# Kernel tuning notes

Measured on AMD Instinct MI355X. Metric: run time of the kernel, lower is better.

## Reference

```python
import jax, jax.numpy as jnp
import numpy as np
import math

NUM_HEADS = 8
WINDOW = 8  # stage=1


def _windowed_attention(q, kv, Wq, bq, Wk, bk, Wv, bv, Wo, bo):
    B, N, C = q.shape
    H = W = int(math.isqrt(N))
    nh, ws = NUM_HEADS, WINDOW
    hd = C // nh
    scale = hd ** -0.5

    qp = q @ Wq + bq   # (B, N, C)
    kp = kv @ Wk + bk
    vp = kv @ Wv + bv

    def to_windows(x):
        # (B, N, C) -> (B, nh, nWh*nWw, ws*ws, hd)
        x = x.reshape(B, H // ws, ws, W // ws, ws, nh, hd)
        x = x.transpose(0, 5, 1, 3, 2, 4, 6)  # B, nh, nWh, nWw, ws, ws, hd
        return x.reshape(B, nh, (H // ws) * (W // ws), ws * ws, hd)

    qw = to_windows(qp)
    kw = to_windows(kp)
    vw = to_windows(vp)

    attn = jnp.einsum('bhnqd,bhnkd->bhnqk', qw, kw) * scale
    attn = jax.nn.softmax(attn.astype(jnp.float32), axis=-1).astype(qw.dtype)
    ow = jnp.einsum('bhnqk,bhnkd->bhnqd', attn, vw)

    # window reverse: (B, nh, nW, ws*ws, hd) -> (B, N, C)
    ow = ow.reshape(B, nh, H // ws, W // ws, ws, ws, hd)
    ow = ow.transpose(0, 2, 4, 3, 5, 1, 6)  # B, nWh, ws, nWw, ws, nh, hd
    x = ow.reshape(B, N, C)

    return x @ Wo + bo


def setup_inputs() -> dict:
    key = jax.random.key(0)
    ks = jax.random.split(key, 7)
    B, N, C = 4, 16384, 256
    s = 1.0 / math.sqrt(C)
    return {
        'q': jax.random.normal(ks[0], (B, N, C), jnp.float32),
        'kv': jax.random.normal(ks[1], (B, N, C), jnp.float32),
        'Wq': jax.random.normal(ks[2], (C, C), jnp.float32) * s,
        'bq': jnp.zeros((C,), jnp.float32),
        'Wk': jax.random.normal(ks[3], (C, C), jnp.float32) * s,
        'bk': jnp.zeros((C,), jnp.float32),
        'Wv': jax.random.normal(ks[4], (C, C), jnp.float32) * s,
        'bv': jnp.zeros((C,), jnp.float32),
        'Wo': jax.random.normal(ks[5], (C, C), jnp.float32) * s,
        'bo': jnp.zeros((C,), jnp.float32),
    }


def reference(q, kv, Wq, bq, Wk, bk, Wv, bv, Wo, bo):
    return _windowed_attention(q, kv, Wq, bq, Wk, bk, Wv, bv, Wo, bo)
```

## Files before the change

### kernel.cpp

```cpp
#include <hip/hip_runtime.h>
#include <hip/hip_bf16.h>

typedef __bf16 bf16;
typedef __bf16 bf16x8 __attribute__((ext_vector_type(8)));
typedef float  f32x4  __attribute__((ext_vector_type(4)));

#define DEVINL __device__ __forceinline__

DEVINL void gll16(const void* g, void* l) {
  __builtin_amdgcn_global_load_lds(
      (const __attribute__((address_space(1))) unsigned int*)g,
      (__attribute__((address_space(3))) unsigned int*)l, 16, 0, 0);
}

__global__ void k_prep(const float* __restrict__ Wq, const float* __restrict__ Wk,
                       const float* __restrict__ Wv, const float* __restrict__ Wo,
                       bf16* __restrict__ wtq_h, bf16* __restrict__ wtq_l,
                       bf16* __restrict__ wtkv_h, bf16* __restrict__ wtkv_l,
                       bf16* __restrict__ wto_h, bf16* __restrict__ wto_l) {
  const int k = blockIdx.x;
  const int n = threadIdx.x;
  const int m = blockIdx.y;
  const float* src = (m == 0) ? Wq : (m == 1) ? Wk : (m == 2) ? Wv : Wo;
  bf16* dh = (m == 0) ? wtq_h : (m == 3) ? wto_h : (m == 1) ? wtkv_h : (wtkv_h + 256 * 256);
  bf16* dl = (m == 0) ? wtq_l : (m == 3) ? wto_l : (m == 1) ? wtkv_l : (wtkv_l + 256 * 256);
  const float v = src[k * 256 + n];
  const bf16 h = (bf16)v;
  dh[n * 256 + k] = h;
  dl[n * 256 + k] = (bf16)(v - (float)h);
}

template <bool ABF16, bool OUTF32>
__global__ __launch_bounds__(256) void k_gemm3(
    const void* __restrict__ Aptr,
    const bf16* __restrict__ Wth, const bf16* __restrict__ Wtl,
    const float* __restrict__ bias0, const float* __restrict__ bias1,
    void* __restrict__ out0, void* __restrict__ out1) {
  __shared__ __align__(16) bf16 Ash[128 * 32];
  __shared__ __align__(16) bf16 Asl[128 * 32];
  __shared__ __align__(16) bf16 Bsh[128 * 32];
  __shared__ __align__(16) bf16 Bsl[128 * 32];

  const int tid = threadIdx.x;
  const int lane = tid & 63;
  const int wave = tid >> 6;
  const int m0 = blockIdx.x * 128;
  const int n0 = blockIdx.y * 128;
  const int mw = (wave >> 1) * 64;
  const int nw = (wave & 1) * 64;
  const int lm = lane & 15;
  const int lq = lane >> 4;

  f32x4 acc[4][4];
#pragma unroll
  for (int i = 0; i < 4; ++i)
#pragma unroll
    for (int j = 0; j < 4; ++j) acc[i][j] = (f32x4)0.0f;

  const int c0 = wave * 128 + lane;
  const int c1 = c0 + 64;
  const int rB0 = c0 >> 2, oB0 = (c0 & 3) * 8;
  const int rB1 = c1 >> 2, oB1 = (c1 & 3) * 8;

  const int rowA = tid >> 1;
  const int halfA = (tid & 1) * 16;

  for (int k0 = 0; k0 < 256; k0 += 32) {
    gll16(Wth + (size_t)(n0 + rB0) * 256 + k0 + oB0, &Bsh[c0 * 8]);
    gll16(Wth + (size_t)(n0 + rB1) * 256 + k0 + oB1, &Bsh[c1 * 8]);
    gll16(Wtl + (size_t)(n0 + rB0) * 256 + k0 + oB0, &Bsl[c0 * 8]);
    gll16(Wtl + (size_t)(n0 + rB1) * 256 + k0 + oB1, &Bsl[c1 * 8]);

    if (ABF16) {
      const bf16* Ab = (const bf16*)Aptr;
      gll16(Ab + (size_t)(m0 + rB0) * 256 + k0 + oB0, &Ash[c0 * 8]);
      gll16(Ab + (size_t)(m0 + rB1) * 256 + k0 + oB1, &Ash[c1 * 8]);
    } else {
      const float* Af = (const float*)Aptr;
      const float* src = Af + (size_t)(m0 + rowA) * 256 + k0 + halfA;
      float4 f0 = *(const float4*)(src);
      float4 f1 = *(const float4*)(src + 4);
      float4 f2 = *(const float4*)(src + 8);
      float4 f3 = *(const float4*)(src + 12);
      bf16x8 h0, l0, h1, l1;
      const float fa[16] = {f0.x, f0.y, f0.z, f0.w, f1.x, f1.y, f1.z, f1.w,
                            f2.x, f2.y, f2.z, f2.w, f3.x, f3.y, f3.z, f3.w};
#pragma unroll
      for (int j = 0; j < 8; ++j) {
        bf16 h = (bf16)fa[j];
        h0[j] = h;
        l0[j] = (bf16)(fa[j] - (float)h);
      }
#pragma unroll
      for (int j = 0; j < 8; ++j) {
        bf16 h = (bf16)fa[8 + j];
        h1[j] = h;
        l1[j] = (bf16)(fa[8 + j] - (float)h);
      }
      const int o = rowA * 32 + halfA;
      *(bf16x8*)&Ash[o] = h0;
      *(bf16x8*)&Ash[o + 8] = h1;
      *(bf16x8*)&Asl[o] = l0;
      *(bf16x8*)&Asl[o + 8] = l1;
    }
    __syncthreads();

    bf16x8 avh[4], bvh[4], bvl[4];
#pragma unroll
    for (int t = 0; t < 4; ++t)
      avh[t] = *(const bf16x8*)&Ash[(mw + t * 16 + lm) * 32 + lq * 8];
#pragma unroll
    for (int t = 0; t < 4; ++t) {
      bvh[t] = *(const bf16x8*)&Bsh[(nw + t * 16 + lm) * 32 + lq * 8];
      bvl[t] = *(const bf16x8*)&Bsl[(nw + t * 16 + lm) * 32 + lq * 8];
    }
#pragma unroll
    for (int i = 0; i < 4; ++i)
#pragma unroll
      for (int j = 0; j < 4; ++j) {
        acc[i][j] = __builtin_amdgcn_mfma_f32_16x16x32_bf16(avh[i], bvh[j], acc[i][j], 0, 0, 0);
        acc[i][j] = __builtin_amdgcn_mfma_f32_16x16x32_bf16(avh[i], bvl[j], acc[i][j], 0, 0, 0);
      }
    if (!ABF16) {
      bf16x8 avl[4];
#pragma unroll
      for (int t = 0; t < 4; ++t)
        avl[t] = *(const bf16x8*)&Asl[(mw + t * 16 + lm) * 32 + lq * 8];
#pragma unroll
      for (int i = 0; i < 4; ++i)
#pragma unroll
        for (int j = 0; j < 4; ++j)
          acc[i][j] = __builtin_amdgcn_mfma_f32_16x16x32_bf16(avl[i], bvh[j], acc[i][j], 0, 0, 0);
    }
    __syncthreads();
  }

#pragma unroll
  for (int i = 0; i < 4; ++i) {
#pragma unroll
    for (int j = 0; j < 4; ++j) {
      const int n_g = n0 + nw + j * 16 + lm;
      const bool hi = (n_g >= 256);
      const float* bp = hi ? bias1 : bias0;
      const int nc = n_g & 255;
      const float bval = bp[nc];
#pragma unroll
      for (int r = 0; r < 4; ++r) {
        const int m_g = m0 + mw + i * 16 + lq * 4 + r;
        const float v = acc[i][j][r] + bval;
        if (OUTF32) {
          float* op = hi ? (float*)out1 : (float*)out0;
          op[(size_t)m_g * 256 + nc] = v;
        } else {
          bf16* op = hi ? (bf16*)out1 : (bf16*)out0;
          op[(size_t)m_g * 256 + nc] = (bf16)v;
        }
      }
    }
  }
}

__global__ __launch_bounds__(256) void k_attn(
    const bf16* __restrict__ qp, const bf16* __restrict__ kp,
    const bf16* __restrict__ vp, bf16* __restrict__ ao) {
  __shared__ __align__(16) bf16 smem[3 * 64 * 136];
  bf16* Qs = smem;
  bf16* Ks = smem + 64 * 136;
  bf16* Vs = smem + 2 * 64 * 136;
  bf16* Ps = smem;
  bf16* Os = Vs;

  const int tid = threadIdx.x;
  const int lane = tid & 63;
  const int hl = tid >> 6;
  const int bw = blockIdx.x;
  const int b = bw >> 8;
  const int w = bw & 255;
  const int wy = w >> 4, wx = w & 15;
  const int ch0 = blockIdx.y * 128;

#pragma unroll
  for (int i = 0; i < 4; ++i) {
    const int c = i * 256 + tid;
    const int t = c >> 4;
    const int off = (c & 15) * 8;
    const int ty = t >> 3, tx = t & 7;
    const size_t gr = ((size_t)(b * 128 + wy * 8 + ty)) * 128 + wx * 8 + tx;
    const size_t gi = gr * 256 + ch0 + off;
    const int li = t * 136 + off;
    *(uint4*)&Qs[li] = *(const uint4*)&qp[gi];
    *(uint4*)&Ks[li] = *(const uint4*)&kp[gi];
    *(uint4*)&Vs[li] = *(const uint4*)&vp[gi];
  }
  __syncthreads();

  const int chh = hl * 32;
  const int lm = lane & 15;
  const int lq = lane >> 4;

  bf16x8 qa[4], kb[4];
#pragma unroll
  for (int t = 0; t < 4; ++t)
    qa[t] = *(const bf16x8*)&Qs[(t * 16 + lm) * 136 + chh + lq * 8];
#pragma unroll
  for (int t = 0; t < 4; ++t)
    kb[t] = *(const bf16x8*)&Ks[(t * 16 + lm) * 136 + chh + lq * 8];

  f32x4 s[4][4];
#pragma unroll
  for (int i = 0; i < 4; ++i)
#pragma unroll
    for (int j = 0; j < 4; ++j) s[i][j] = (f32x4)0.0f;
#pragma unroll
  for (int i = 0; i < 4; ++i)
#pragma unroll
    for (int j = 0; j < 4; ++j)
      s[i][j] = __builtin_amdgcn_mfma_f32_16x16x32_bf16(qa[i], kb[j], s[i][j], 0, 0, 0);

  const float scale = 0.17677669529663687f;
  float rl[4][4];
#pragma unroll
  for (int mt = 0; mt < 4; ++mt) {
#pragma unroll
    for (int r = 0; r < 4; ++r) {
      float mx = fmaxf(fmaxf(s[mt][0][r], s[mt][1][r]), fmaxf(s[mt][2][r], s[mt][3][r]));
      mx = fmaxf(mx, __shfl_xor(mx, 1));
      mx = fmaxf(mx, __shfl_xor(mx, 2));
      mx = fmaxf(mx, __shfl_xor(mx, 4));
      mx = fmaxf(mx, __shfl_xor(mx, 8));
      float sum = 0.f;
#pragma unroll
      for (int nt = 0; nt < 4; ++nt) {
        const float p = __expf((s[mt][nt][r] - mx) * scale);
        s[mt][nt][r] = p;
        sum += p;
      }
      sum += __shfl_xor(sum, 1);
      sum += __shfl_xor(sum, 2);
      sum += __shfl_xor(sum, 4);
      sum += __shfl_xor(sum, 8);
      rl[mt][r] = 1.0f / sum;
    }
  }

  __syncthreads();

  bf16* Ph = Ps + hl * 4096;
#pragma unroll
  for (int mt = 0; mt < 4; ++mt)
#pragma unroll
    for (int nt = 0; nt < 4; ++nt)
#pragma unroll
      for (int r = 0; r < 4; ++r) {
        const int qrow = mt * 16 + lq * 4 + r;
        const int kcol = nt * 16 + lm;
        Ph[qrow * 64 + (((kcol >> 3) ^ (qrow & 7)) << 3) + (kcol & 7)] = (bf16)s[mt][nt][r];
      }

  f32x4 o[4][2];
#pragma unroll
  for (int i = 0; i < 4; ++i) { o[i][0] = (f32x4)0.0f; o[i][1] = (f32x4)0.0f; }
#pragma unroll
  for (int ks = 0; ks < 2; ++ks) {
    bf16x8 pa[4];
#pragma unroll
    for (int mt = 0; mt < 4; ++mt) {
      const int qrow = mt * 16 + lm;
      const int g = ks * 4 + lq;
      pa[mt] = *(const bf16x8*)&Ph[qrow * 64 + ((g ^ (qrow & 7)) << 3)];
    }
    bf16x8 vbf[2];
#pragma unroll
    for (int ntd = 0; ntd < 2; ++ntd) {
      const int d = ntd * 16 + lm;
      bf16x8 tv;
#pragma unroll
      for (int j = 0; j < 8; ++j)
        tv[j] = Vs[(ks * 32 + lq * 8 + j) * 136 + chh + d];
      vbf[ntd] = tv;
    }
#pragma unroll
    for (int mt = 0; mt < 4; ++mt)
#pragma unroll
      for (int ntd = 0; ntd < 2; ++ntd)
        o[mt][ntd] = __builtin_amdgcn_mfma_f32_16x16x32_bf16(pa[mt], vbf[ntd], o[mt][ntd], 0, 0, 0);
  }

  __syncthreads();

#pragma unroll
  for (int mt = 0; mt < 4; ++mt)
#pragma unroll
    for (int ntd = 0; ntd < 2; ++ntd)
#pragma unroll
      for (int r = 0; r < 4; ++r) {
        const int qrow = mt * 16 + lq * 4 + r;
        const int d = ntd * 16 + lm;
        Os[qrow * 136 + chh + d] = (bf16)(o[mt][ntd][r] * rl[mt][r]);
      }
  __syncthreads();

#pragma unroll
  for (int i = 0; i < 4; ++i) {
    const int c = i * 256 + tid;
    const int t = c >> 4;
    const int off = (c & 15) * 8;
    const int ty = t >> 3, tx = t & 7;
    const size_t gr = ((size_t)(b * 128 + wy * 8 + ty)) * 128 + wx * 8 + tx;
    *(uint4*)&ao[gr * 256 + ch0 + off] = *(const uint4*)&Os[t * 136 + off];
  }
}

extern "C" void kernel_launch(void* const* d_in, const int* in_sizes, int n_in,
                              void* d_out, int out_size, void* d_ws, size_t ws_size,
                              hipStream_t stream) {
  const float* q  = (const float*)d_in[0];
  const float* kv = (const float*)d_in[1];
  const float* Wq = (const float*)d_in[2];
  const float* bq = (const float*)d_in[3];
  const float* Wk = (const float*)d_in[4];
  const float* bk = (const float*)d_in[5];
  const float* Wv = (const float*)d_in[6];
  const float* bv = (const float*)d_in[7];
  const float* Wo = (const float*)d_in[8];
  const float* bo = (const float*)d_in[9];
  float* out = (float*)d_out;

  char* ws = (char*)d_ws;
  bf16* wtq_h  = (bf16*)(ws + 0);
  bf16* wtq_l  = (bf16*)(ws + 131072);
  bf16* wtkv_h = (bf16*)(ws + 262144);
  bf16* wtkv_l = (bf16*)(ws + 524288);
  bf16* wto_h  = (bf16*)(ws + 786432);
  bf16* wto_l  = (bf16*)(ws + 917504);
  const size_t PLANE = (size_t)65536 * 256 * 2;
  bf16* qp = (bf16*)(ws + 1048576);
  bf16* kp = (bf16*)(ws + 1048576 + PLANE);
  bf16* vp = (bf16*)(ws + 1048576 + 2 * PLANE);
  bf16* ao = (bf16*)(ws + 1048576 + 3 * PLANE);
  if (ws_size < 1048576 + 4 * PLANE) return;

  k_prep<<<dim3(256, 4), 256, 0, stream>>>(Wq, Wk, Wv, Wo, wtq_h, wtq_l,
                                           wtkv_h, wtkv_l, wto_h, wto_l);
  k_gemm3<false, false><<<dim3(512, 2), 256, 0, stream>>>(
      (const void*)q, wtq_h, wtq_l, bq, bq, (void*)qp, (void*)qp);
  k_gemm3<false, false><<<dim3(512, 4), 256, 0, stream>>>(
      (const void*)kv, wtkv_h, wtkv_l, bk, bv, (void*)kp, (void*)vp);
  k_attn<<<dim3(1024, 2), 256, 0, stream>>>(qp, kp, vp, ao);
  k_gemm3<true, true><<<dim3(512, 2), 256, 0, stream>>>(
      (const void*)ao, wto_h, wto_l, bo, bo, (void*)out, (void*)out);
}
```

Baseline: 323.6 us.

## Fuse QKV projections, drop activation low-part split, use 64-row tiles with XCD mapping

Replaces the templated GEMM with a fused Q/K/V projection kernel and a dedicated output projection kernel. The fp32 activations are now rounded to a single bf16 term, removing the low-part split and one third of the MFMAs. Tiles shrink to 64 rows, and block indices are remapped so neighbouring rows spread across XCDs, with higher occupancy hints. This trades some accuracy in the projections for less compute and fewer launches.

After: 329.4 us. About the same (+1.8%).

```diff
diff --git a/kernel.cpp b/kernel.cpp
--- a/kernel.cpp
+++ b/kernel.cpp
@@ -11,6 +11,13 @@
   __builtin_amdgcn_global_load_lds(
       (const __attribute__((address_space(1))) unsigned int*)g,
       (__attribute__((address_space(3))) unsigned int*)l, 16, 0, 0);
+}
+
+DEVINL bf16x8 cvt_hi(const float4& a, const float4& b) {
+  bf16x8 h;
+  h[0] = (bf16)a.x; h[1] = (bf16)a.y; h[2] = (bf16)a.z; h[3] = (bf16)a.w;
+  h[4] = (bf16)b.x; h[5] = (bf16)b.y; h[6] = (bf16)b.z; h[7] = (bf16)b.w;
+  return h;
 }
 
 __global__ void k_prep(const float* __restrict__ Wq, const float* __restrict__ Wk,
@@ -30,131 +37,174 @@
   dl[n * 256 + k] = (bf16)(v - (float)h);
 }
 
-template <bool ABF16, bool OUTF32>
-__global__ __launch_bounds__(256) void k_gemm3(
-    const void* __restrict__ Aptr,
-    const bf16* __restrict__ Wth, const bf16* __restrict__ Wtl,
-    const float* __restrict__ bias0, const float* __restrict__ bias1,
-    void* __restrict__ out0, void* __restrict__ out1) {
-  __shared__ __align__(16) bf16 Ash[128 * 32];
-  __shared__ __align__(16) bf16 Asl[128 * 32];
+__global__ __launch_bounds__(256, 4) void k_qkv(
+    const float* __restrict__ q, const float* __restrict__ kv,
+    const bf16* __restrict__ wtq_h, const bf16* __restrict__ wtq_l,
+    const bf16* __restrict__ wtkv_h, const bf16* __restrict__ wtkv_l,
+    const float* __restrict__ bq, const float* __restrict__ bk,
+    const float* __restrict__ bv,
+    bf16* __restrict__ qp, bf16* __restrict__ kp, bf16* __restrict__ vp) {
+  __shared__ __align__(16) bf16 Ash[64 * 32];
   __shared__ __align__(16) bf16 Bsh[128 * 32];
   __shared__ __align__(16) bf16 Bsl[128 * 32];
+
+  const int g = blockIdx.x;
+  const int xcd = g & 7;
+  const int s = g >> 3;
+  const int nb = s % 6;
+  const int mh = s / 6;
+  const int m0 = (mh * 8 + xcd) * 64;
+
+  const bool isq = (nb < 2);
+  const float* A = isq ? q : kv;
+  const bf16* Wh = isq ? wtq_h : wtkv_h;
+  const bf16* Wl = isq ? wtq_l : wtkv_l;
+  const int n0 = isq ? nb * 128 : (nb - 2) * 128;
 
   const int tid = threadIdx.x;
   const int lane = tid & 63;
   const int wave = tid >> 6;
-  const int m0 = blockIdx.x * 128;
-  const int n0 = blockIdx.y * 128;
-  const int mw = (wave >> 1) * 64;
+  const int mw = (wave >> 1) * 32;
   const int nw = (wave & 1) * 64;
   const int lm = lane & 15;
   const int lq = lane >> 4;
 
-  f32x4 acc[4][4];
-#pragma unroll
-  for (int i = 0; i < 4; ++i)
+  f32x4 acc[2][4];
+#pragma unroll
+  for (int i = 0; i < 2; ++i)
 #pragma unroll
     for (int j = 0; j < 4; ++j) acc[i][j] = (f32x4)0.0f;
 
-  const int c0 = wave * 128 + lane;
-  const int c1 = c0 + 64;
-  const int rB0 = c0 >> 2, oB0 = (c0 & 3) * 8;
-  const int rB1 = c1 >> 2, oB1 = (c1 & 3) * 8;
-
-  const int rowA = tid >> 1;
-  const int halfA = (tid & 1) * 16;
+  const int rB0 = tid >> 2, oB0 = (tid & 3) * 8;
+  const int rB1 = (tid + 256) >> 2, oB1 = oB0;
+  const int rowA = tid >> 2;
+  const int qA = (tid & 3) * 8;
 
   for (int k0 = 0; k0 < 256; k0 += 32) {
-    gll16(Wth + (size_t)(n0 + rB0) * 256 + k0 + oB0, &Bsh[c0 * 8]);
-    gll16(Wth + (size_t)(n0 + rB1) * 256 + k0 + oB1, &Bsh[c1 * 8]);
-    gll16(Wtl + (size_t)(n0 + rB0) * 256 + k0 + oB0, &Bsl[c0 * 8]);
-    gll16(Wtl + (size_t)(n0 + rB1) * 256 + k0 + oB1, &Bsl[c1 * 8]);
-
-    if (ABF16) {
-      const bf16* Ab = (const bf16*)Aptr;
-      gll16(Ab + (size_t)(m0 + rB0) * 256 + k0 + oB0, &Ash[c0 * 8]);
-      gll16(Ab + (size_t)(m0 + rB1) * 256 + k0 + oB1, &Ash[c1 * 8]);
-    } else {
-      const float* Af = (const float*)Aptr;
-      const float* src = Af + (size_t)(m0 + rowA) * 256 + k0 + halfA;
-      float4 f0 = *(const float4*)(src);
-      float4 f1 = *(const float4*)(src + 4);
-      float4 f2 = *(const float4*)(src + 8);
-      float4 f3 = *(const float4*)(src + 12);
-      bf16x8 h0, l0, h1, l1;
-      const float fa[16] = {f0.x, f0.y, f0.z, f0.w, f1.x, f1.y, f1.z, f1.w,
-                            f2.x, f2.y, f2.z, f2.w, f3.x, f3.y, f3.z, f3.w};
-#pragma unroll
-      for (int j = 0; j < 8; ++j) {
-        bf16 h = (bf16)fa[j];
-        h0[j] = h;
-        l0[j] = (bf16)(fa[j] - (float)h);
-      }
-#pragma unroll
-      for (int j = 0; j < 8; ++j) {
-        bf16 h = (bf16)fa[8 + j];
-        h1[j] = h;
-        l1[j] = (bf16)(fa[8 + j] - (float)h);
-      }
-      const int o = rowA * 32 + halfA;
-      *(bf16x8*)&Ash[o] = h0;
-      *(bf16x8*)&Ash[o + 8] = h1;
-      *(bf16x8*)&Asl[o] = l0;
-      *(bf16x8*)&Asl[o + 8] = l1;
-    }
+    gll16(Wh + (size_t)(n0 + rB0) * 256 + k0 + oB0, &Bsh[tid * 8]);
+    gll16(Wh + (size_t)(n0 + rB1) * 256 + k0 + oB1, &Bsh[(tid + 256) * 8]);
+    gll16(Wl + (size_t)(n0 + rB0) * 256 + k0 + oB0, &Bsl[tid * 8]);
+    gll16(Wl + (size_t)(n0 + rB1) * 256 + k0 + oB1, &Bsl[(tid + 256) * 8]);
+
+    const float* src = A + (size_t)(m0 + rowA) * 256 + k0 + qA;
+    const float4 f0 = *(const float4*)(src);
+    const float4 f1 = *(const float4*)(src + 4);
+    *(bf16x8*)&Ash[rowA * 32 + qA] = cvt_hi(f0, f1);
     __syncthreads();
 
-    bf16x8 avh[4], bvh[4], bvl[4];
-#pragma unroll
-    for (int t = 0; t < 4; ++t)
-      avh[t] = *(const bf16x8*)&Ash[(mw + t * 16 + lm) * 32 + lq * 8];
-#pragma unroll
-    for (int t = 0; t < 4; ++t) {
-      bvh[t] = *(const bf16x8*)&Bsh[(nw + t * 16 + lm) * 32 + lq * 8];
-      bvl[t] = *(const bf16x8*)&Bsl[(nw + t * 16 + lm) * 32 + lq * 8];
-    }
-#pragma unroll
-    for (int i = 0; i < 4; ++i)
+    bf16x8 av[2], bh[4], bl[4];
+#pragma unroll
+    for (int t = 0; t < 2; ++t)
+      av[t] = *(const bf16x8*)&Ash[(mw + t * 16 + lm) * 32 + lq * 8];
+#pragma unroll
+    for (int j = 0; j < 4; ++j) {
+      bh[j] = *(const bf16x8*)&Bsh[(nw + j * 16 + lm) * 32 + lq * 8];
+      bl[j] = *(const bf16x8*)&Bsl[(nw + j * 16 + lm) * 32 + lq * 8];
+    }
+#pragma unroll
+    for (int i = 0; i < 2; ++i)
 #pragma unroll
       for (int j = 0; j < 4; ++j) {
-        acc[i][j] = __builtin_amdgcn_mfma_f32_16x16x32_bf16(avh[i], bvh[j], acc[i][j], 0, 0, 0);
-        acc[i][j] = __builtin_amdgcn_mfma_f32_16x16x32_bf16(avh[i], bvl[j], acc[i][j], 0, 0, 0);
-      }
-    if (!ABF16) {
-      bf16x8 avl[4];
-#pragma unroll
-      for (int t = 0; t < 4; ++t)
-        avl[t] = *(const bf16x8*)&Asl[(mw + t * 16 + lm) * 32 + lq * 8];
-#pragma unroll
-      for (int i = 0; i < 4; ++i)
-#pragma unroll
-        for (int j = 0; j < 4; ++j)
-          acc[i][j] = __builtin_amdgcn_mfma_f32_16x16x32_bf16(avl[i], bvh[j], acc[i][j], 0, 0, 0);
-    }
+        acc[i][j] = __builtin_amdgcn_mfma_f32_16x16x32_bf16(av[i], bh[j], acc[i][j], 0, 0, 0);
+        acc[i][j] = __builtin_amdgcn_mfma_f32_16x16x32_bf16(av[i], bl[j], acc[i][j], 0, 0, 0);
+      }
     __syncthreads();
   }
 
 #pragma unroll
-  for (int i = 0; i < 4; ++i) {
+  for (int i = 0; i < 2; ++i) {
 #pragma unroll
     for (int j = 0; j < 4; ++j) {
       const int n_g = n0 + nw + j * 16 + lm;
-      const bool hi = (n_g >= 256);
-      const float* bp = hi ? bias1 : bias0;
-      const int nc = n_g & 255;
-      const float bval = bp[nc];
+      bf16* op;
+      float bval;
+      int nc;
+      if (isq) {
+        op = qp; nc = n_g; bval = bq[n_g];
+      } else if (n_g < 256) {
+        op = kp; nc = n_g; bval = bk[n_g];
+      } else {
+        op = vp; nc = n_g - 256; bval = bv[n_g - 256];
+      }
 #pragma unroll
       for (int r = 0; r < 4; ++r) {
         const int m_g = m0 + mw + i * 16 + lq * 4 + r;
-        const float v = acc[i][j][r] + bval;
-        if (OUTF32) {
-          float* op = hi ? (float*)out1 : (float*)out0;
-          op[(size_t)m_g * 256 + nc] = v;
-        } else {
-          bf16* op = hi ? (bf16*)out1 : (bf16*)out0;
-          op[(size_t)m_g * 256 + nc] = (bf16)v;
-        }
+        op[(size_t)m_g * 256 + nc] = (bf16)(acc[i][j][r] + bval);
+      }
+    }
+  }
+}
+
+__global__ __launch_bounds__(256, 4) void k_oproj(
+    const bf16* __restrict__ A, const bf16* __restrict__ Wh,
+    const bf16* __restrict__ Wl, const float* __restrict__ bias,
+    float* __restrict__ out) {
+  __shared__ __align__(16) bf16 Ash[64 * 32];
+  __shared__ __align__(16) bf16 Bsh[128 * 32];
+  __shared__ __align__(16) bf16 Bsl[128 * 32];
+
+  const int g = blockIdx.x;
+  const int xcd = g & 7;
+  const int s = g >> 3;
+  const int nb = s & 1;
+  const int mh = s >> 1;
+  const int m0 = (mh * 8 + xcd) * 64;
+  const int n0 = nb * 128;
+
+  const int tid = threadIdx.x;
+  const int lane = tid & 63;
+  const int wave = tid >> 6;
+  const int mw = (wave >> 1) * 32;
+  const int nw = (wave & 1) * 64;
+  const int lm = lane & 15;
+  const int lq = lane >> 4;
+
+  f32x4 acc[2][4];
+#pragma unroll
+  for (int i = 0; i < 2; ++i)
+#pragma unroll
+    for (int j = 0; j < 4; ++j) acc[i][j] = (f32x4)0.0f;
+
+  const int rB0 = tid >> 2, oB0 = (tid & 3) * 8;
+  const int rB1 = (tid + 256) >> 2;
+
+  for (int k0 = 0; k0 < 256; k0 += 32) {
+    gll16(Wh + (size_t)(n0 + rB0) * 256 + k0 + oB0, &Bsh[tid * 8]);
+    gll16(Wh + (size_t)(n0 + rB1) * 256 + k0 + oB0, &Bsh[(tid + 256) * 8]);
+    gll16(Wl + (size_t)(n0 + rB0) * 256 + k0 + oB0, &Bsl[tid * 8]);
+    gll16(Wl + (size_t)(n0 + rB1) * 256 + k0 + oB0, &Bsl[(tid + 256) * 8]);
+    gll16(A + (size_t)(m0 + rB0) * 256 + k0 + oB0, &Ash[tid * 8]);
+    __syncthreads();
+
+    bf16x8 av[2], bh[4], bl[4];
+#pragma unroll
+    for (int t = 0; t < 2; ++t)
+      av[t] = *(const bf16x8*)&Ash[(mw + t * 16 + lm) * 32 + lq * 8];
+#pragma unroll
+    for (int j = 0; j < 4; ++j) {
+      bh[j] = *(const bf16x8*)&Bsh[(nw + j * 16 + lm) * 32 + lq * 8];
+      bl[j] = *(const bf16x8*)&Bsl[(nw + j * 16 + lm) * 32 + lq * 8];
+    }
+#pragma unroll
+    for (int i = 0; i < 2; ++i)
+#pragma unroll
+      for (int j = 0; j < 4; ++j) {
+        acc[i][j] = __builtin_amdgcn_mfma_f32_16x16x32_bf16(av[i], bh[j], acc[i][j], 0, 0, 0);
+        acc[i][j] = __builtin_amdgcn_mfma_f32_16x16x32_bf16(av[i], bl[j], acc[i][j], 0, 0, 0);
+      }
+    __syncthreads();
+  }
+
+#pragma unroll
+  for (int i = 0; i < 2; ++i) {
+#pragma unroll
+    for (int j = 0; j < 4; ++j) {
+      const int n_g = n0 + nw + j * 16 + lm;
+      const float bval = bias[n_g];
+#pragma unroll
+      for (int r = 0; r < 4; ++r) {
+        const int m_g = m0 + mw + i * 16 + lq * 4 + r;
+        out[(size_t)m_g * 256 + n_g] = acc[i][j][r] + bval;
       }
     }
   }
@@ -266,8 +316,8 @@
 #pragma unroll
     for (int mt = 0; mt < 4; ++mt) {
       const int qrow = mt * 16 + lm;
-      const int g = ks * 4 + lq;
-      pa[mt] = *(const bf16x8*)&Ph[qrow * 64 + ((g ^ (qrow & 7)) << 3)];
+      const int gsel = ks * 4 + lq;
+      pa[mt] = *(const bf16x8*)&Ph[qrow * 64 + ((gsel ^ (qrow & 7)) << 3)];
     }
     bf16x8 vbf[2];
 #pragma unroll
@@ -342,11 +392,8 @@
 
   k_prep<<<dim3(256, 4), 256, 0, stream>>>(Wq, Wk, Wv, Wo, wtq_h, wtq_l,
                                            wtkv_h, wtkv_l, wto_h, wto_l);
-  k_gemm3<false, false><<<dim3(512, 2), 256, 0, stream>>>(
-      (const void*)q, wtq_h, wtq_l, bq, bq, (void*)qp, (void*)qp);
-  k_gemm3<false, false><<<dim3(512, 4), 256, 0, stream>>>(
-      (const void*)kv, wtkv_h, wtkv_l, bk, bv, (void*)kp, (void*)vp);
+  k_qkv<<<6144, 256, 0, stream>>>(q, kv, wtq_h, wtq_l, wtkv_h, wtkv_l,
+                                  bq, bk, bv, qp, kp, vp);
   k_attn<<<dim3(1024, 2), 256, 0, stream>>>(qp, kp, vp, ao);
-  k_gemm3<true, true><<<dim3(512, 2), 256, 0, stream>>>(
-      (const void*)ao, wto_h, wto_l, bo, bo, (void*)out, (void*)out);
-}
+  k_oproj<<<2048, 256, 0, stream>>>(ao, wto_h, wto_l, bo, out);
+}
```

## Drop split-bf16 compensation in QKV, pre-pack weights, fuse QKV GEMM launches

Applied to the files above, without the earlier changes.

The Q/K/V projections now use plain bf16 inputs and weights instead of the hi/lo split with three MFMAs per tile, and the separate Q and KV GEMMs become one kernel with XCD-aware block mapping. Weights are pre-packed into a tile-contiguous layout so B tiles are staged with straight global_load_lds copies. K is now processed 64 at a time per barrier pair. The output projection keeps compensation only on the weights, as an extra K-range of the packed layout. The intent is to cut MFMA work and launch count, at the cost of lower projection precision that could affect the tolerance check.

Measured after the change: 311.4 us. 1.04x faster.

```diff
diff --git a/kernel.cpp b/kernel.cpp
--- a/kernel.cpp
+++ b/kernel.cpp
@@ -15,149 +15,182 @@
 
 __global__ void k_prep(const float* __restrict__ Wq, const float* __restrict__ Wk,
                        const float* __restrict__ Wv, const float* __restrict__ Wo,
-                       bf16* __restrict__ wtq_h, bf16* __restrict__ wtq_l,
-                       bf16* __restrict__ wtkv_h, bf16* __restrict__ wtkv_l,
-                       bf16* __restrict__ wto_h, bf16* __restrict__ wto_l) {
+                       bf16* __restrict__ packQ, bf16* __restrict__ packO) {
+  const int n = threadIdx.x;
   const int k = blockIdx.x;
-  const int n = threadIdx.x;
   const int m = blockIdx.y;
-  const float* src = (m == 0) ? Wq : (m == 1) ? Wk : (m == 2) ? Wv : Wo;
-  bf16* dh = (m == 0) ? wtq_h : (m == 3) ? wto_h : (m == 1) ? wtkv_h : (wtkv_h + 256 * 256);
-  bf16* dl = (m == 0) ? wtq_l : (m == 3) ? wto_l : (m == 1) ? wtkv_l : (wtkv_l + 256 * 256);
-  const float v = src[k * 256 + n];
-  const bf16 h = (bf16)v;
-  dh[n * 256 + k] = h;
-  dl[n * 256 + k] = (bf16)(v - (float)h);
-}
-
-template <bool ABF16, bool OUTF32>
-__global__ __launch_bounds__(256) void k_gemm3(
-    const void* __restrict__ Aptr,
-    const bf16* __restrict__ Wth, const bf16* __restrict__ Wtl,
-    const float* __restrict__ bias0, const float* __restrict__ bias1,
-    void* __restrict__ out0, void* __restrict__ out1) {
-  __shared__ __align__(16) bf16 Ash[128 * 32];
-  __shared__ __align__(16) bf16 Asl[128 * 32];
-  __shared__ __align__(16) bf16 Bsh[128 * 32];
-  __shared__ __align__(16) bf16 Bsl[128 * 32];
-
-  const int tid = threadIdx.x;
-  const int lane = tid & 63;
-  const int wave = tid >> 6;
-  const int m0 = blockIdx.x * 128;
-  const int n0 = blockIdx.y * 128;
-  const int mw = (wave >> 1) * 64;
-  const int nw = (wave & 1) * 64;
-  const int lm = lane & 15;
-  const int lq = lane >> 4;
+  const int kk = k & 63, iter4 = k >> 6;
+  const int h = kk >> 5, kg = (kk >> 3) & 3, e = k & 7;
+  if (m < 3) {
+    const float* W = (m == 0) ? Wq : (m == 1) ? Wk : Wv;
+    const bf16 v = (bf16)W[k * 256 + n];
+    const int nglob = m * 256 + n;
+    const int tile = nglob >> 7, row = nglob & 127;
+    packQ[(size_t)((tile * 4 + iter4) * 1024 + h * 512 + row * 4 + kg) * 8 + e] = v;
+  } else {
+    const float w = Wo[k * 256 + n];
+    const bf16 hi = (bf16)w;
+    const bf16 v = (m == 3) ? hi : (bf16)(w - (float)hi);
+    const int iter = (m - 3) * 4 + iter4;
+    const int tile = n >> 7, row = n & 127;
+    packO[(size_t)((tile * 8 + iter) * 1024 + h * 512 + row * 4 + kg) * 8 + e] = v;
+  }
+}
+
+__global__ __launch_bounds__(256, 3) void k_qkv(
+    const float* __restrict__ q, const float* __restrict__ kv,
+    const bf16* __restrict__ packQ,
+    const float* __restrict__ bq, const float* __restrict__ bk,
+    const float* __restrict__ bvv,
+    bf16* __restrict__ qp, bf16* __restrict__ kp, bf16* __restrict__ vp) {
+  __shared__ __align__(16) bf16 As[2][128 * 32];
+  __shared__ __align__(16) bf16 Bs[2][128 * 32];
+
+  const int g = blockIdx.x, xcd = g & 7, s = g >> 3;
+  const int nb = s % 6, mh = s / 6;
+  const int m0 = (mh * 8 + xcd) * 128;
+  const float* A = (nb < 2) ? q : kv;
+
+  const int tid = threadIdx.x, lane = tid & 63, wave = tid >> 6;
+  const int mw = (wave >> 1) * 64, nw = (wave & 1) * 64;
+  const int lm = lane & 15, lq = lane >> 4;
 
   f32x4 acc[4][4];
 #pragma unroll
-  for (int i = 0; i < 4; ++i)
-#pragma unroll
-    for (int j = 0; j < 4; ++j) acc[i][j] = (f32x4)0.0f;
-
-  const int c0 = wave * 128 + lane;
-  const int c1 = c0 + 64;
-  const int rB0 = c0 >> 2, oB0 = (c0 & 3) * 8;
-  const int rB1 = c1 >> 2, oB1 = (c1 & 3) * 8;
+  for (int a = 0; a < 4; ++a)
+#pragma unroll
+    for (int b = 0; b < 4; ++b) acc[a][b] = (f32x4)0.0f;
 
   const int rowA = tid >> 1;
-  const int halfA = (tid & 1) * 16;
-
-  for (int k0 = 0; k0 < 256; k0 += 32) {
-    gll16(Wth + (size_t)(n0 + rB0) * 256 + k0 + oB0, &Bsh[c0 * 8]);
-    gll16(Wth + (size_t)(n0 + rB1) * 256 + k0 + oB1, &Bsh[c1 * 8]);
-    gll16(Wtl + (size_t)(n0 + rB0) * 256 + k0 + oB0, &Bsl[c0 * 8]);
-    gll16(Wtl + (size_t)(n0 + rB1) * 256 + k0 + oB1, &Bsl[c1 * 8]);
-
-    if (ABF16) {
-      const bf16* Ab = (const bf16*)Aptr;
-      gll16(Ab + (size_t)(m0 + rB0) * 256 + k0 + oB0, &Ash[c0 * 8]);
-      gll16(Ab + (size_t)(m0 + rB1) * 256 + k0 + oB1, &Ash[c1 * 8]);
-    } else {
-      const float* Af = (const float*)Aptr;
-      const float* src = Af + (size_t)(m0 + rowA) * 256 + k0 + halfA;
-      float4 f0 = *(const float4*)(src);
-      float4 f1 = *(const float4*)(src + 4);
-      float4 f2 = *(const float4*)(src + 8);
-      float4 f3 = *(const float4*)(src + 12);
-      bf16x8 h0, l0, h1, l1;
-      const float fa[16] = {f0.x, f0.y, f0.z, f0.w, f1.x, f1.y, f1.z, f1.w,
-                            f2.x, f2.y, f2.z, f2.w, f3.x, f3.y, f3.z, f3.w};
-#pragma unroll
-      for (int j = 0; j < 8; ++j) {
-        bf16 h = (bf16)fa[j];
-        h0[j] = h;
-        l0[j] = (bf16)(fa[j] - (float)h);
-      }
-#pragma unroll
-      for (int j = 0; j < 8; ++j) {
-        bf16 h = (bf16)fa[8 + j];
-        h1[j] = h;
-        l1[j] = (bf16)(fa[8 + j] - (float)h);
-      }
-      const int o = rowA * 32 + halfA;
-      *(bf16x8*)&Ash[o] = h0;
-      *(bf16x8*)&Ash[o + 8] = h1;
-      *(bf16x8*)&Asl[o] = l0;
-      *(bf16x8*)&Asl[o + 8] = l1;
+  const int hA = tid & 1;
+  const bf16* pbase = packQ + (size_t)nb * 4 * 8192;
+
+  for (int i = 0; i < 4; ++i) {
+    const bf16* pit = pbase + i * 8192;
+#pragma unroll
+    for (int u = 0; u < 4; ++u) {
+      const int c = u * 256 + tid;
+      bf16* dst = (u < 2) ? &Bs[0][c * 8] : &Bs[1][(c - 512) * 8];
+      gll16(pit + c * 8, dst);
+    }
+    const float* srcA = A + (size_t)(m0 + rowA) * 256 + i * 64 + hA * 32;
+    bf16* dstA = &As[hA][rowA * 32];
+#pragma unroll
+    for (int half = 0; half < 2; ++half) {
+      const float4 f0 = *(const float4*)(srcA + half * 16 + 0);
+      const float4 f1 = *(const float4*)(srcA + half * 16 + 4);
+      const float4 f2 = *(const float4*)(srcA + half * 16 + 8);
+      const float4 f3 = *(const float4*)(srcA + half * 16 + 12);
+      bf16x8 b0, b1;
+      b0[0] = (bf16)f0.x; b0[1] = (bf16)f0.y; b0[2] = (bf16)f0.z; b0[3] = (bf16)f0.w;
+      b0[4] = (bf16)f1.x; b0[5] = (bf16)f1.y; b0[6] = (bf16)f1.z; b0[7] = (bf16)f1.w;
+      b1[0] = (bf16)f2.x; b1[1] = (bf16)f2.y; b1[2] = (bf16)f2.z; b1[3] = (bf16)f2.w;
+      b1[4] = (bf16)f3.x; b1[5] = (bf16)f3.y; b1[6] = (bf16)f3.z; b1[7] = (bf16)f3.w;
+      *(bf16x8*)&dstA[half * 16] = b0;
+      *(bf16x8*)&dstA[half * 16 + 8] = b1;
     }
     __syncthreads();
-
-    bf16x8 avh[4], bvh[4], bvl[4];
-#pragma unroll
-    for (int t = 0; t < 4; ++t)
-      avh[t] = *(const bf16x8*)&Ash[(mw + t * 16 + lm) * 32 + lq * 8];
-#pragma unroll
-    for (int t = 0; t < 4; ++t) {
-      bvh[t] = *(const bf16x8*)&Bsh[(nw + t * 16 + lm) * 32 + lq * 8];
-      bvl[t] = *(const bf16x8*)&Bsl[(nw + t * 16 + lm) * 32 + lq * 8];
-    }
-#pragma unroll
-    for (int i = 0; i < 4; ++i)
-#pragma unroll
-      for (int j = 0; j < 4; ++j) {
-        acc[i][j] = __builtin_amdgcn_mfma_f32_16x16x32_bf16(avh[i], bvh[j], acc[i][j], 0, 0, 0);
-        acc[i][j] = __builtin_amdgcn_mfma_f32_16x16x32_bf16(avh[i], bvl[j], acc[i][j], 0, 0, 0);
-      }
-    if (!ABF16) {
-      bf16x8 avl[4];
+#pragma unroll
+    for (int ks = 0; ks < 2; ++ks) {
+      bf16x8 av[4], bvf[4];
 #pragma unroll
       for (int t = 0; t < 4; ++t)
-        avl[t] = *(const bf16x8*)&Asl[(mw + t * 16 + lm) * 32 + lq * 8];
-#pragma unroll
-      for (int i = 0; i < 4; ++i)
-#pragma unroll
-        for (int j = 0; j < 4; ++j)
-          acc[i][j] = __builtin_amdgcn_mfma_f32_16x16x32_bf16(avl[i], bvh[j], acc[i][j], 0, 0, 0);
+        av[t] = *(const bf16x8*)&As[ks][(mw + t * 16 + lm) * 32 + lq * 8];
+#pragma unroll
+      for (int t = 0; t < 4; ++t)
+        bvf[t] = *(const bf16x8*)&Bs[ks][(nw + t * 16 + lm) * 32 + lq * 8];
+#pragma unroll
+      for (int a = 0; a < 4; ++a)
+#pragma unroll
+        for (int b = 0; b < 4; ++b)
+          acc[a][b] = __builtin_amdgcn_mfma_f32_16x16x32_bf16(av[a], bvf[b], acc[a][b], 0, 0, 0);
     }
     __syncthreads();
   }
 
 #pragma unroll
-  for (int i = 0; i < 4; ++i) {
-#pragma unroll
-    for (int j = 0; j < 4; ++j) {
-      const int n_g = n0 + nw + j * 16 + lm;
-      const bool hi = (n_g >= 256);
-      const float* bp = hi ? bias1 : bias0;
-      const int nc = n_g & 255;
+  for (int a = 0; a < 4; ++a)
+#pragma unroll
+    for (int b = 0; b < 4; ++b) {
+      const int nglob = nb * 128 + nw + b * 16 + lm;
+      bf16* op; const float* bp; int nc;
+      if (nglob < 256)      { op = qp; nc = nglob;       bp = bq; }
+      else if (nglob < 512) { op = kp; nc = nglob - 256; bp = bk; }
+      else                  { op = vp; nc = nglob - 512; bp = bvv; }
       const float bval = bp[nc];
 #pragma unroll
       for (int r = 0; r < 4; ++r) {
-        const int m_g = m0 + mw + i * 16 + lq * 4 + r;
-        const float v = acc[i][j][r] + bval;
-        if (OUTF32) {
-          float* op = hi ? (float*)out1 : (float*)out0;
-          op[(size_t)m_g * 256 + nc] = v;
-        } else {
-          bf16* op = hi ? (bf16*)out1 : (bf16*)out0;
-          op[(size_t)m_g * 256 + nc] = (bf16)v;
-        }
-      }
-    }
-  }
+        const int mg = m0 + mw + a * 16 + lq * 4 + r;
+        op[(size_t)mg * 256 + nc] = (bf16)(acc[a][b][r] + bval);
+      }
+    }
+}
+
+__global__ __launch_bounds__(256, 3) void k_oproj(
+    const bf16* __restrict__ ao, const bf16* __restrict__ packO,
+    const float* __restrict__ bo, float* __restrict__ out) {
+  __shared__ __align__(16) bf16 As[2][128 * 32];
+  __shared__ __align__(16) bf16 Bs[2][128 * 32];
+
+  const int g = blockIdx.x, xcd = g & 7, s = g >> 3;
+  const int nb = s & 1, mh = s >> 1;
+  const int m0 = (mh * 8 + xcd) * 128;
+
+  const int tid = threadIdx.x, lane = tid & 63, wave = tid >> 6;
+  const int mw = (wave >> 1) * 64, nw = (wave & 1) * 64;
+  const int lm = lane & 15, lq = lane >> 4;
+
+  f32x4 acc[4][4];
+#pragma unroll
+  for (int a = 0; a < 4; ++a)
+#pragma unroll
+    for (int b = 0; b < 4; ++b) acc[a][b] = (f32x4)0.0f;
+
+  const bf16* pbase = packO + (size_t)nb * 8 * 8192;
+
+  for (int i = 0; i < 8; ++i) {
+    const int kA = (i & 3) * 64;
+#pragma unroll
+    for (int u = 0; u < 4; ++u) {
+      const int c = u * 256 + tid;
+      const int h = c >> 9, r2 = c & 511;
+      const int row = r2 >> 2, kg = c & 3;
+      bf16* dstB = (u < 2) ? &Bs[0][c * 8] : &Bs[1][(c - 512) * 8];
+      gll16(pbase + (size_t)i * 8192 + c * 8, dstB);
+      bf16* dstA = (u < 2) ? &As[0][r2 * 8] : &As[1][r2 * 8];
+      gll16(ao + (size_t)(m0 + row) * 256 + kA + h * 32 + kg * 8, dstA);
+    }
+    __syncthreads();
+#pragma unroll
+    for (int ks = 0; ks < 2; ++ks) {
+      bf16x8 av[4], bvf[4];
+#pragma unroll
+      for (int t = 0; t < 4; ++t)
+        av[t] = *(const bf16x8*)&As[ks][(mw + t * 16 + lm) * 32 + lq * 8];
+#pragma unroll
+      for (int t = 0; t < 4; ++t)
+        bvf[t] = *(const bf16x8*)&Bs[ks][(nw + t * 16 + lm) * 32 + lq * 8];
+#pragma unroll
+      for (int a = 0; a < 4; ++a)
+#pragma unroll
+        for (int b = 0; b < 4; ++b)
+          acc[a][b] = __builtin_amdgcn_mfma_f32_16x16x32_bf16(av[a], bvf[b], acc[a][b], 0, 0, 0);
+    }
+    __syncthreads();
+  }
+
+#pragma unroll
+  for (int a = 0; a < 4; ++a)
+#pragma unroll
+    for (int b = 0; b < 4; ++b) {
+      const int nglob = nb * 128 + nw + b * 16 + lm;
+      const float bval = bo[nglob];
+#pragma unroll
+      for (int r = 0; r < 4; ++r) {
+        const int mg = m0 + mw + a * 16 + lq * 4 + r;
+        out[(size_t)mg * 256 + nglob] = acc[a][b][r] + bval;
+      }
+    }
 }
 
 __global__ __launch_bounds__(256) void k_attn(
@@ -266,8 +299,8 @@
 #pragma unroll
     for (int mt = 0; mt < 4; ++mt) {
       const int qrow = mt * 16 + lm;
-      const int g = ks * 4 + lq;
-      pa[mt] = *(const bf16x8*)&Ph[qrow * 64 + ((g ^ (qrow & 7)) << 3)];
+      const int gsel = ks * 4 + lq;
+      pa[mt] = *(const bf16x8*)&Ph[qrow * 64 + ((gsel ^ (qrow & 7)) << 3)];
     }
     bf16x8 vbf[2];
 #pragma unroll
@@ -327,12 +360,8 @@
   float* out = (float*)d_out;
 
   char* ws = (char*)d_ws;
-  bf16* wtq_h  = (bf16*)(ws + 0);
-  bf16* wtq_l  = (bf16*)(ws + 131072);
-  bf16* wtkv_h = (bf16*)(ws + 262144);
-  bf16* wtkv_l = (bf16*)(ws + 524288);
-  bf16* wto_h  = (bf16*)(ws + 786432);
-  bf16* wto_l  = (bf16*)(ws + 917504);
+  bf16* packQ = (bf16*)(ws + 0);
+  bf16* packO = (bf16*)(ws + 393216);
   const size_t PLANE = (size_t)65536 * 256 * 2;
   bf16* qp = (bf16*)(ws + 1048576);
   bf16* kp = (bf16*)(ws + 1048576 + PLANE);
@@ -340,13 +369,8 @@
   bf16* ao = (bf16*)(ws + 1048576 + 3 * PLANE);
   if (ws_size < 1048576 + 4 * PLANE) return;
 
-  k_prep<<<dim3(256, 4), 256, 0, stream>>>(Wq, Wk, Wv, Wo, wtq_h, wtq_l,
-                                           wtkv_h, wtkv_l, wto_h, wto_l);
-  k_gemm3<false, false><<<dim3(512, 2), 256, 0, stream>>>(
-      (const void*)q, wtq_h, wtq_l, bq, bq, (void*)qp, (void*)qp);
-  k_gemm3<false, false><<<dim3(512, 4), 256, 0, stream>>>(
-      (const void*)kv, wtkv_h, wtkv_l, bk, bv, (void*)kp, (void*)vp);
+  k_prep<<<dim3(256, 5), 256, 0, stream>>>(Wq, Wk, Wv, Wo, packQ, packO);
+  k_qkv<<<3072, 256, 0, stream>>>(q, kv, packQ, bq, bk, bv, qp, kp, vp);
   k_attn<<<dim3(1024, 2), 256, 0, stream>>>(qp, kp, vp, ao);
-  k_gemm3<true, true><<<dim3(512, 2), 256, 0, stream>>>(
-      (const void*)ao, wto_h, wto_l, bo, bo, (void*)out, (void*)out);
-}
+  k_oproj<<<1024, 256, 0, stream>>>(ao, packO, bo, out);
+}
```
